# Kernel tuning notes

Measured on AMD Instinct MI355X. Metric: run time of the kernel, lower is better.

The kernel has to match this reference:

```python
import jax, jax.numpy as jnp
import numpy as np

# dims
B, L, H, NH, D = 512, 200, 128, 4, 32      # batch, seq_len, hidden, heads (gnn & fcb), head dim H/NH
FT, TP, IP = 32, 64, 200                    # first_taxonomy_num, taxonomy/item nodes per graph
NHOP, NB = 2, 2                             # n_hop gnn layers, gip_block_nums
SH, FH = 512, 256                           # scb_hidden_units, fcb_hidden_units
ITEMS, TAX = 100001, 2000                   # item vocab (+pad row 0), taxonomy vocab
NT, NI = B * TP, B * IP                     # total taxonomy / item nodes in batched forest
DEG_I, DEG_T = 4, 2                         # in-degree per taxonomy node for i2t / t2t edges


def _ln(x, g, b, eps=1e-8):
    m = jnp.mean(x, -1, keepdims=True)
    v = jnp.mean((x - m) ** 2, -1, keepdims=True)
    return (x - m) / jnp.sqrt(v + eps) * g + b


def _gat(src_h, dst_h, es, ed, W, al, ar, bias):
    """DGL GATConv (eval mode): shared fc, leaky_relu(0.2) scores, segment softmax,
    identity residual (in == heads*out), bias, ReLU activation."""
    fs = (src_h @ W).reshape(-1, NH, D)                 # [Ns,NH,D]
    fd = (dst_h @ W).reshape(-1, NH, D)                 # [Nd,NH,D]
    el = jnp.sum(fs * al, -1)                           # [Ns,NH]
    er = jnp.sum(fd * ar, -1)                           # [Nd,NH]
    e = jax.nn.leaky_relu(el[es] + er[ed], 0.2)         # [E,NH]
    emax = jax.ops.segment_max(e, ed, num_segments=NT)
    a = jnp.exp(e - emax[ed])
    s = jax.ops.segment_sum(a, ed, num_segments=NT)
    alpha = a / s[ed]                                   # [E,NH]
    rst = jax.ops.segment_sum(alpha[..., None] * fs[es], ed, num_segments=NT)
    rst = rst + dst_h.reshape(-1, NH, D) + bias.reshape(NH, D)
    return jax.nn.relu(rst).reshape(-1, NH * D)


def _forward(item_embed, tax_embed, scb_ln_g, scb_ln_b, scb_w1, scb_w2, fcb_ln_g, fcb_ln_b,
             fcb_w1, fcb_w2, fcb_w3, wv, gi_w, gi_al, gi_ar, gi_b, gt_w, gt_al, gt_ar, gt_b,
             liw_g, liw_b, int_g, int_b, uni_w,
             seq, root, i2t_src, i2t_dst, t2t_src, t2t_dst, item_ids, tax_ids):
    # --- global intention: mixer-style blocks over the item sequence ---
    V = item_embed[seq]                                           # [B,L,H]
    for i in range(NB):
        nv = _ln(V, scb_ln_g[i], scb_ln_b[i])
        t = jax.nn.gelu(jnp.einsum('blh,ls->bhs', nv, scb_w1[i]), approximate=False)
        vs = nv + jnp.einsum('bhs,sl->blh', t, scb_w2[i])         # seq-mixing block
        nvs = _ln(vs, fcb_ln_g[i], fcb_ln_b[i])
        xh = nvs.reshape(B, L, NH, D)                             # fcb heads share w1/w2
        y = jax.nn.gelu(jnp.einsum('blkc,cf->blkf', xh, fcb_w1[i]), approximate=False)
        y = jnp.einsum('blkf,fc->blkc', y, fcb_w2[i]).reshape(B, L, H)
        V = nvs + y @ fcb_w3[i]
    alpha = jax.nn.softmax(V @ wv, axis=1)                        # [B,L]
    g = jnp.sum(alpha[..., None] * V, axis=1)                     # [B,H]
    # --- local intention: multi-hop hetero GAT on batched item-taxonomy forest ---
    item_h = item_embed[item_ids]                                 # [NI,H]
    tax_h = tax_embed[tax_ids]                                    # [NT,H]
    acc = jnp.zeros_like(tax_h)
    for hop in range(NHOP):
        t_i = _gat(item_h, tax_h, i2t_src, i2t_dst, gi_w[hop], gi_al[hop], gi_ar[hop], gi_b[hop])
        t_t = _gat(tax_h, tax_h, t2t_src, t2t_dst, gt_w[hop], gt_al[hop], gt_ar[hop], gt_b[hop])
        tax_h = t_i + t_t                                         # HeteroGraphConv 'sum'
        acc = acc + tax_h                                         # k_list accumulation
    total = acc / NHOP                                            # average over hops
    offs = jnp.arange(B) * TP                                     # batched-graph offsets (graph_taxonomy)
    valid = root != -1
    local = jnp.where(valid[..., None], total[jnp.clip(root, 0) + offs[:, None]], 0.0)  # [B,FT,H]
    # --- fuse global + local ---
    mul = jnp.einsum('bfh,bh->bf', local, g)                      # [B,FT]
    w = jax.nn.softmax(jnp.where(mul != 0, _ln(mul, liw_g, liw_b), -jnp.inf), axis=-1)
    intention = _ln(g + jnp.sum(w[..., None] * local, axis=1), int_g, int_b)
    return (intention @ uni_w) @ item_embed.T                     # [B, ITEMS]


def setup_inputs():
    key = jax.random.key(0)
    ks = jax.random.split(key, 32)
    nrm = lambda i, sh: jax.random.normal(ks[i], sh, jnp.float32) * 0.05
    inp = {}
    inp['seq'] = jax.random.randint(ks[0], (B, L), 0, ITEMS)
    inp['root'] = jax.random.randint(ks[1], (B, FT), 0, TP)       # all valid roots
    i2t_dst = jnp.repeat(jnp.arange(NT), DEG_I)
    inp['i2t_dst'] = i2t_dst
    inp['i2t_src'] = (i2t_dst // TP) * IP + jax.random.randint(ks[2], (NT * DEG_I,), 0, IP)
    t2t_dst = jnp.repeat(jnp.arange(NT), DEG_T)
    inp['t2t_dst'] = t2t_dst
    inp['t2t_src'] = (t2t_dst // TP) * TP + jax.random.randint(ks[3], (NT * DEG_T,), 0, TP)
    inp['item_ids'] = jax.random.randint(ks[4], (NI,), 1, ITEMS)
    inp['tax_ids'] = jax.random.randint(ks[5], (NT,), 1, TAX)
    inp['item_embed'] = nrm(6, (ITEMS, H)).at[0].set(0.0)         # padding_idx=0
    inp['tax_embed'] = nrm(7, (TAX, H)).at[0].set(0.0)
    inp['scb_ln_g'] = jnp.ones((NB, H)); inp['scb_ln_b'] = jnp.zeros((NB, H))
    inp['scb_w1'] = nrm(8, (NB, L, SH)); inp['scb_w2'] = nrm(9, (NB, SH, L))
    inp['fcb_ln_g'] = jnp.ones((NB, H)); inp['fcb_ln_b'] = jnp.zeros((NB, H))
    inp['fcb_w1'] = nrm(10, (NB, D, FH)); inp['fcb_w2'] = nrm(11, (NB, FH, D))
    inp['fcb_w3'] = nrm(12, (NB, H, H))
    inp['wv'] = nrm(13, (H,))
    inp['gi_w'] = nrm(14, (NHOP, H, H)); inp['gi_al'] = nrm(15, (NHOP, NH, D))
    inp['gi_ar'] = nrm(16, (NHOP, NH, D)); inp['gi_b'] = nrm(17, (NHOP, H))
    inp['gt_w'] = nrm(18, (NHOP, H, H)); inp['gt_al'] = nrm(19, (NHOP, NH, D))
    inp['gt_ar'] = nrm(20, (NHOP, NH, D)); inp['gt_b'] = nrm(21, (NHOP, H))
    inp['liw_g'] = jnp.ones((FT,)); inp['liw_b'] = jnp.zeros((FT,))
    inp['int_g'] = jnp.ones((H,)); inp['int_b'] = jnp.zeros((H,))
    inp['uni_w'] = nrm(22, (H, H))
    return inp


def reference(item_embed, tax_embed, scb_ln_g, scb_ln_b, scb_w1, scb_w2, fcb_ln_g, fcb_ln_b,
              fcb_w1, fcb_w2, fcb_w3, wv, gi_w, gi_al, gi_ar, gi_b, gt_w, gt_al, gt_ar, gt_b,
              liw_g, liw_b, int_g, int_b, uni_w,
              seq, root, i2t_src, i2t_dst, t2t_src, t2t_dst, item_ids, tax_ids):
    return _forward(item_embed, tax_embed, scb_ln_g, scb_ln_b, scb_w1, scb_w2, fcb_ln_g, fcb_ln_b,
                    fcb_w1, fcb_w2, fcb_w3, wv, gi_w, gi_al, gi_ar, gi_b, gt_w, gt_al, gt_ar, gt_b,
                    liw_g, liw_b, int_g, int_b, uni_w,
                    seq, root, i2t_src, i2t_dst, t2t_src, t2t_dst, item_ids, tax_ids)
```

## Files before the change

### kernel.cpp

```cpp
#include <hip/hip_runtime.h>
#include <hip/hip_bf16.h>

constexpr int TB = 512, TL = 200, TH = 128, TNH = 4, TD = 32;
constexpr int TFT = 32, TTP = 64, TIP = 200;
constexpr int TSH = 512, TFH = 256;
constexpr int TITEMS = 100001;
constexpr int TNT = TB * TTP;
constexpr int TNI = TB * TIP;
constexpr int TLP = 224;
constexpr int TIPAD = 100096;

typedef __attribute__((ext_vector_type(8))) short short8v;
typedef __attribute__((ext_vector_type(4))) float f32x4;

__device__ inline float gelu_exact(float x) {
    return 0.5f * x * (1.0f + erff(x * 0.7071067811865476f));
}
__device__ inline float gelu_fast(float x) {
    float u = x + 0.044715f * x * x * x;
    float e = exp2f(-2.302208f * u);
    return x / (1.0f + e);
}
__device__ inline unsigned short to_bf16u(float x) {
    __hip_bfloat16 h = __float2bfloat16(x);
    return *reinterpret_cast<unsigned short*>(&h);
}
__device__ inline float bfu_to_f(unsigned short u) {
    unsigned int x = ((unsigned int)u) << 16;
    return __uint_as_float(x);
}

__device__ inline float block_reduce_sum(float v, float* red) {
    for (int o = 32; o > 0; o >>= 1) v += __shfl_down(v, o, 64);
    int nw = blockDim.x >> 6;
    if ((threadIdx.x & 63) == 0) red[threadIdx.x >> 6] = v;
    __syncthreads();
    float r = 0.f;
    for (int w = 0; w < nw; ++w) r += red[w];
    __syncthreads();
    return r;
}

__device__ inline float block_reduce_max(float v, float* red) {
    for (int o = 32; o > 0; o >>= 1) v = fmaxf(v, __shfl_down(v, o, 64));
    int nw = blockDim.x >> 6;
    if ((threadIdx.x & 63) == 0) red[threadIdx.x >> 6] = v;
    __syncthreads();
    float r = -INFINITY;
    for (int w = 0; w < nw; ++w) r = fmaxf(r, red[w]);
    __syncthreads();
    return r;
}

__global__ __launch_bounds__(256) void k_gather(const float* __restrict__ tab,
                                                const int* __restrict__ idx,
                                                float* __restrict__ out, int nrows) {
    int e = blockIdx.x * blockDim.x + threadIdx.x;
    if (e >= nrows * 32) return;
    int r = e >> 5, c = e & 31;
    ((float4*)out)[e] = ((const float4*)tab)[(size_t)idx[r] * 32 + c];
}

__global__ __launch_bounds__(256) void k_gather_bf(const float* __restrict__ tab,
                                                   const int* __restrict__ idx,
                                                   unsigned short* __restrict__ out, int nrows) {
    int e = blockIdx.x * blockDim.x + threadIdx.x;
    if (e >= nrows * 16) return;
    int r = e >> 4, c = e & 15;
    const float4 a = ((const float4*)tab)[(size_t)idx[r] * 32 + c * 2];
    const float4 b = ((const float4*)tab)[(size_t)idx[r] * 32 + c * 2 + 1];
    uint4 u;
    u.x = (unsigned int)to_bf16u(a.x) | ((unsigned int)to_bf16u(a.y) << 16);
    u.y = (unsigned int)to_bf16u(a.z) | ((unsigned int)to_bf16u(a.w) << 16);
    u.z = (unsigned int)to_bf16u(b.x) | ((unsigned int)to_bf16u(b.y) << 16);
    u.w = (unsigned int)to_bf16u(b.z) | ((unsigned int)to_bf16u(b.w) << 16);
    *(uint4*)(out + (size_t)e * 8) = u;
}

__global__ __launch_bounds__(256) void k_wcvt(const float* __restrict__ fw1, const float* __restrict__ fw2,
                                              const float* __restrict__ fw3, const float* __restrict__ giw,
                                              const float* __restrict__ gtw, unsigned short* __restrict__ WB) {
    int idx = blockIdx.x * 256 + threadIdx.x;
    float v;
    if (idx < 16384) {
        int nb = idx >> 13, r = idx & 8191, n = r >> 5, k = r & 31;
        v = fw1[(size_t)nb * 8192 + k * 256 + n];
    } else if (idx < 32768) {
        int t = idx - 16384;
        int nb = t >> 13, r = t & 8191, n = r >> 8, k = r & 255;
        v = fw2[(size_t)nb * 8192 + k * 32 + n];
    } else if (idx < 65536) {
        int t = idx - 32768;
        int nb = t >> 14, r = t & 16383, n = r >> 7, k = r & 127;
        v = fw3[(size_t)nb * 16384 + k * 128 + n];
    } else if (idx < 98304) {
        int t = idx - 65536;
        int hop = t >> 14, r = t & 16383, n = r >> 7, k = r & 127;
        v = giw[(size_t)hop * 16384 + k * 128 + n];
    } else {
        int t = idx - 98304;
        int hop = t >> 14, r = t & 16383, n = r >> 7, k = r & 127;
        v = gtw[(size_t)hop * 16384 + k * 128 + n];
    }
    WB[idx] = to_bf16u(v);
}

__global__ __launch_bounds__(256) void k_ln(const float* __restrict__ x, float* __restrict__ y,
                                            const float* __restrict__ g, const float* __restrict__ b) {
    int row = blockIdx.x * 8 + (threadIdx.x >> 5);
    int lane = threadIdx.x & 31;
    const float4 v = ((const float4*)(x + (size_t)row * TH))[lane];
    float s = v.x + v.y + v.z + v.w;
    for (int o = 16; o > 0; o >>= 1) s += __shfl_down(s, o, 32);
    float mean = __shfl(s, 0, 32) * (1.f / 128.f);
    float4 d;
    d.x = v.x - mean; d.y = v.y - mean; d.z = v.z - mean; d.w = v.w - mean;
    float q = d.x * d.x + d.y * d.y + d.z * d.z + d.w * d.w;
    for (int o = 16; o > 0; o >>= 1) q += __shfl_down(q, o, 32);
    float inv = rsqrtf(__shfl(q, 0, 32) * (1.f / 128.f) + 1e-8f);
    const float4 gg = ((const float4*)g)[lane];
    const float4 bb = ((const float4*)b)[lane];
    float4 o4;
    o4.x = d.x * inv * gg.x + bb.x;
    o4.y = d.y * inv * gg.y + bb.y;
    o4.z = d.z * inv * gg.z + bb.z;
    o4.w = d.w * inv * gg.w + bb.w;
    ((float4*)(y + (size_t)row * TH))[lane] = o4;
}

__global__ __launch_bounds__(128) void k_nvt(const float* __restrict__ NV,
                                             unsigned short* __restrict__ NVT) {
    __shared__ float tl[64][129];
    int b = blockIdx.y, l0 = blockIdx.x * 64, tid = threadIdx.x;
    for (int i = tid; i < 2048; i += 128) {
        int r = i >> 5, c = i & 31;
        int l = l0 + r;
        float4 v = {0.f, 0.f, 0.f, 0.f};
        if (l < TL) v = *(const float4*)(NV + ((size_t)b * TL + l) * TH + c * 4);
        tl[r][c * 4 + 0] = v.x; tl[r][c * 4 + 1] = v.y;
        tl[r][c * 4 + 2] = v.z; tl[r][c * 4 + 3] = v.w;
    }
    __syncthreads();
    int h = tid;
    int ng = (l0 + 64 > TLP) ? (TLP - l0) / 8 : 8;
    for (int lg = 0; lg < ng; ++lg) {
        uint4 u;
        unsigned int p[4];
#pragma unroll
        for (int q = 0; q < 4; ++q) {
            unsigned short ua = to_bf16u(tl[lg * 8 + q * 2 + 0][h]);
            unsigned short ub = to_bf16u(tl[lg * 8 + q * 2 + 1][h]);
            p[q] = (unsigned int)ua | ((unsigned int)ub << 16);
        }
        u.x = p[0]; u.y = p[1]; u.z = p[2]; u.w = p[3];
        *(uint4*)(NVT + ((size_t)b * TH + h) * TLP + l0 + lg * 8) = u;
    }
}

__global__ __launch_bounds__(256) void k_wscb(const float* __restrict__ w1, const float* __restrict__ w2,
                                              unsigned short* __restrict__ W1T,
                                              unsigned short* __restrict__ W2T) {
    int bx = blockIdx.x;
    if (bx < TSH) {
        int s = bx, l = threadIdx.x;
        if (l < TLP) W1T[(size_t)s * TLP + l] = to_bf16u(l < TL ? w1[(size_t)l * TSH + s] : 0.f);
    } else {
        int l = bx - TSH;
        for (int it = 0; it < 2; ++it) {
            int s = it * 256 + threadIdx.x;
            W2T[(size_t)l * TSH + s] = to_bf16u(l < TL ? w2[(size_t)s * TL + l] : 0.f);
        }
    }
}

__global__ __launch_bounds__(256) void k_mm1(const unsigned short* __restrict__ NVT,
                                             const unsigned short* __restrict__ W1T,
                                             unsigned short* __restrict__ T, int bh) {
    __shared__ unsigned short As[128][40];
    __shared__ unsigned short Bs[128][40];
    int tid = threadIdx.x;
    int b_local = blockIdx.y, b = bh * 256 + b_local;
    int s0 = blockIdx.x * 128;
    int lane = tid & 63, wid = tid >> 6;
    int mw = wid >> 1, nw = wid & 1;
    f32x4 acc[4][4];
#pragma unroll
    for (int i = 0; i < 4; ++i)
#pragma unroll
        for (int j = 0; j < 4; ++j) acc[i][j] = (f32x4){0.f, 0.f, 0.f, 0.f};
    const unsigned short* Abase = NVT + (size_t)b * TH * TLP;
    const unsigned short* Bbase = W1T + (size_t)s0 * TLP;
    for (int kc = 0; kc < 7; ++kc) {
        __syncthreads();
        for (int i = tid; i < 512; i += 256) {
            int r = i >> 2, q = i & 3;
            *(uint4*)&As[r][q * 8] = *(const uint4*)(Abase + (size_t)r * TLP + kc * 32 + q * 8);
            *(uint4*)&Bs[r][q * 8] = *(const uint4*)(Bbase + (size_t)r * TLP + kc * 32 + q * 8);
        }
        __syncthreads();
        int ko = (lane >> 4) * 8;
        short8v af[4], bfr[4];
#pragma unroll
        for (int t = 0; t < 4; ++t) {
            af[t] = *(const short8v*)&As[mw * 64 + t * 16 + (lane & 15)][ko];
            bfr[t] = *(const short8v*)&Bs[nw * 64 + t * 16 + (lane & 15)][ko];
        }
#pragma unroll
        for (int i = 0; i < 4; ++i)
#pragma unroll
            for (int j = 0; j < 4; ++j)
                acc[i][j] = __builtin_amdgcn_mfma_f32_16x16x32_bf16(af[i], bfr[j], acc[i][j], 0, 0, 0);
    }
    int rbase = (lane >> 4) * 4, col = lane & 15;
#pragma unroll
    for (int i = 0; i < 4; ++i)
#pragma unroll
        for (int j = 0; j < 4; ++j) {
            int h0 = mw * 64 + i * 16 + rbase;
            int s = s0 + nw * 64 + j * 16 + col;
#pragma unroll
            for (int r = 0; r < 4; ++r)
                T[((size_t)b_local * TH + h0 + r) * TSH + s] = to_bf16u(gelu_fast(acc[i][j][r]));
        }
}

__global__ __launch_bounds__(256) void k_mm2(const unsigned short* __restrict__ T,
                                             const unsigned short* __restrict__ W2T,
                                             const float* __restrict__ NV,
                                             float* __restrict__ VS, int bh) {
    __shared__ unsigned short As[128][40];
    __shared__ unsigned short Bs[64][40];
    int tid = threadIdx.x;
    int b_local = blockIdx.y, b = bh * 256 + b_local;
    int l0 = blockIdx.x * 64;
    int lane = tid & 63, wid = tid >> 6;
    f32x4 acc[2][4];
#pragma unroll
    for (int i = 0; i < 2; ++i)
#pragma unroll
        for (int j = 0; j < 4; ++j) acc[i][j] = (f32x4){0.f, 0.f, 0.f, 0.f};
    const unsigned short* Abase = T + (size_t)b_local * TH * TSH;
    for (int kc = 0; kc < 16; ++kc) {
        __syncthreads();
        for (int i = tid; i < 512; i += 256) {
            int r = i >> 2, q = i & 3;
            *(uint4*)&As[r][q * 8] = *(const uint4*)(Abase + (size_t)r * TSH + kc * 32 + q * 8);
        }
        {
            int r = tid >> 2, q = tid & 3;
            int l = l0 + r;
            uint4 v = {0u, 0u, 0u, 0u};
            if (l < 208) v = *(const uint4*)(W2T + (size_t)l * TSH + kc * 32 + q * 8);
            *(uint4*)&Bs[r][q * 8] = v;
        }
        __syncthreads();
        int ko = (lane >> 4) * 8;
        short8v af[2], bfr[4];
#pragma unroll
        for (int t = 0; t < 2; ++t)
            af[t] = *(const short8v*)&As[wid * 32 + t * 16 + (lane & 15)][ko];
#pragma unroll
        for (int j = 0; j < 4; ++j)
            bfr[j] = *(const short8v*)&Bs[j * 16 + (lane & 15)][ko];
#pragma unroll
        for (int i = 0; i < 2; ++i)
#pragma unroll
            for (int j = 0; j < 4; ++j)
                acc[i][j] = __builtin_amdgcn_mfma_f32_16x16x32_bf16(af[i], bfr[j], acc[i][j], 0, 0, 0);
    }
    int rbase = (lane >> 4) * 4, col = lane & 15;
#pragma unroll
    for (int i = 0; i < 2; ++i)
#pragma unroll
        for (int j = 0; j < 4; ++j) {
            int l = l0 + j * 16 + col;
            if (l < TL) {
                int h0 = wid * 32 + i * 16 + rbase;
                size_t off = ((size_t)b * TL + l) * TH + h0;
                const float4 res = *(const float4*)(NV + off);
                float4 o;
                o.x = acc[i][j][0] + res.x;
                o.y = acc[i][j][1] + res.y;
                o.z = acc[i][j][2] + res.z;
                o.w = acc[i][j][3] + res.w;
                *(float4*)(VS + off) = o;
            }
        }
}

__global__ __launch_bounds__(256) void k_ffuse(const float* __restrict__ NV,
                                               const unsigned short* __restrict__ FW1B,
                                               const unsigned short* __restrict__ FW2B,
                                               unsigned short* __restrict__ Z) {
    __shared__ unsigned short As[64][40];
    __shared__ unsigned short BsBuf[256 * 40];
    __shared__ unsigned short Yl[64 * 264];
    int tid = threadIdx.x;
    int m0 = blockIdx.x * 64;
    int lane = tid & 63, wid = tid >> 6;
    for (int i = tid; i < 512; i += 256) {
        int r = i >> 3, q = i & 7;
        const float4 v = *(const float4*)(NV + (size_t)(m0 + r) * 32 + q * 4);
        ushort4 u;
        u.x = to_bf16u(v.x); u.y = to_bf16u(v.y); u.z = to_bf16u(v.z); u.w = to_bf16u(v.w);
        *(ushort4*)&As[r][q * 4] = u;
    }
    for (int i = tid; i < 1024; i += 256) {
        int r = i >> 2, q = i & 3;
        *(uint4*)&BsBuf[r * 40 + q * 8] = *(const uint4*)(FW1B + r * 32 + q * 8);
    }
    __syncthreads();
    int ko = (lane >> 4) * 8;
    short8v af[4], bfr[4];
#pragma unroll
    for (int t = 0; t < 4; ++t) {
        af[t] = *(const short8v*)&As[t * 16 + (lane & 15)][ko];
        bfr[t] = *(const short8v*)&BsBuf[(wid * 64 + t * 16 + (lane & 15)) * 40 + ko];
    }
    __syncthreads();
    {
        f32x4 acc[4][4];
#pragma unroll
        for (int i = 0; i < 4; ++i)
#pragma unroll
            for (int j = 0; j < 4; ++j) acc[i][j] = (f32x4){0.f, 0.f, 0.f, 0.f};
#pragma unroll
        for (int i = 0; i < 4; ++i)
#pragma unroll
            for (int j = 0; j < 4; ++j)
                acc[i][j] = __builtin_amdgcn_mfma_f32_16x16x32_bf16(af[i], bfr[j], acc[i][j], 0, 0, 0);
        int rbase = (lane >> 4) * 4, col = lane & 15;
#pragma unroll
        for (int i = 0; i < 4; ++i)
#pragma unroll
            for (int j = 0; j < 4; ++j)
#pragma unroll
                for (int r = 0; r < 4; ++r) {
                    int m = i * 16 + rbase + r;
                    int n = wid * 64 + j * 16 + col;
                    int idx = (m * 264 + n) ^ (((m >> 2) & 7) << 3);
                    Yl[idx] = to_bf16u(gelu_fast(acc[i][j][r]));
                }
    }
    for (int i = tid; i < 1024; i += 256) {
        int r = i >> 5, q = i & 31;
        *(uint4*)&BsBuf[r * 264 + q * 8] = *(const uint4*)(FW2B + r * 256 + q * 8);
    }
    __syncthreads();
    {
        f32x4 acc2[2];
        acc2[0] = (f32x4){0.f, 0.f, 0.f, 0.f};
        acc2[1] = (f32x4){0.f, 0.f, 0.f, 0.f};
        int mrow = wid * 16 + (lane & 15);
        int sw = ((mrow >> 2) & 7) << 3;
        for (int kc = 0; kc < 8; ++kc) {
            int ko2 = kc * 32 + (lane >> 4) * 8;
            short8v a2 = *(const short8v*)&Yl[(mrow * 264 + ko2) ^ sw];
            short8v b0 = *(const short8v*)&BsBuf[(lane & 15) * 264 + ko2];
            short8v b1 = *(const short8v*)&BsBuf[(16 + (lane & 15)) * 264 + ko2];
            acc2[0] = __builtin_amdgcn_mfma_f32_16x16x32_bf16(a2, b0, acc2[0], 0, 0, 0);
            acc2[1] = __builtin_amdgcn_mfma_f32_16x16x32_bf16(a2, b1, acc2[1], 0, 0, 0);
        }
        int rbase = (lane >> 4) * 4, col = lane & 15;
#pragma unroll
        for (int j = 0; j < 2; ++j)
#pragma unroll
            for (int r = 0; r < 4; ++r)
                Z[(size_t)(m0 + wid * 16 + rbase + r) * 32 + j * 16 + col] =
                    to_bf16u(acc2[j][r]);
    }
}

__global__ __launch_bounds__(256) void k_gmm_b(const unsigned short* __restrict__ A,
                                               const unsigned short* __restrict__ WB,
                                               const float* __restrict__ R,
                                               float* __restrict__ C) {
    __shared__ unsigned short As[128][40];
    __shared__ unsigned short Bs[128][40];
    int tid = threadIdx.x;
    int m0 = blockIdx.x * 128;
    int lane = tid & 63, wid = tid >> 6;
    int mw = wid >> 1, nw = wid & 1;
    f32x4 acc[4][4];
#pragma unroll
    for (int i = 0; i < 4; ++i)
#pragma unroll
        for (int j = 0; j < 4; ++j) acc[i][j] = (f32x4){0.f, 0.f, 0.f, 0.f};
    for (int kc = 0; kc < 4; ++kc) {
        __syncthreads();
        for (int i = tid; i < 512; i += 256) {
            int r = i >> 2, q = i & 3;
            *(uint4*)&As[r][q * 8] = *(const uint4*)(A + (size_t)(m0 + r) * TH + kc * 32 + q * 8);
            *(uint4*)&Bs[r][q * 8] = *(const uint4*)(WB + (size_t)r * TH + kc * 32 + q * 8);
        }
        __syncthreads();
        int ko = (lane >> 4) * 8;
        short8v af[4], bfr[4];
#pragma unroll
        for (int t = 0; t < 4; ++t) {
            af[t] = *(const short8v*)&As[mw * 64 + t * 16 + (lane & 15)][ko];
            bfr[t] = *(const short8v*)&Bs[nw * 64 + t * 16 + (lane & 15)][ko];
        }
#pragma unroll
        for (int i = 0; i < 4; ++i)
#pragma unroll
            for (int j = 0; j < 4; ++j)
                acc[i][j] = __builtin_amdgcn_mfma_f32_16x16x32_bf16(af[i], bfr[j], acc[i][j], 0, 0, 0);
    }
    int rbase = (lane >> 4) * 4, col = lane & 15;
#pragma unroll
    for (int i = 0; i < 4; ++i)
#pragma unroll
        for (int j = 0; j < 4; ++j) {
            int n = nw * 64 + j * 16 + col;
#pragma unroll
            for (int r = 0; r < 4; ++r) {
                size_t off = (size_t)(m0 + mw * 64 + i * 16 + rbase + r) * TH + n;
                float v = acc[i][j][r];
                if (R) v += R[off];
                C[off] = v;
            }
        }
}

__global__ __launch_bounds__(256) void k_pool(const float* __restrict__ V, const float* __restrict__ wv,
                                              float* __restrict__ g) {
    __shared__ float sc[TL];
    __shared__ float red[4];
    int b = blockIdx.x, tid = threadIdx.x;
    if (tid < TL) {
        float a = 0.f;
        const float* vp = V + (size_t)(b * TL + tid) * TH;
        for (int h = 0; h < TH; ++h) a += vp[h] * wv[h];
        sc[tid] = a;
    }
    __syncthreads();
    float m = (tid < TL) ? sc[tid] : -INFINITY;
    m = block_reduce_max(m, red);
    float e = (tid < TL) ? expf(sc[tid] - m) : 0.f;
    float s = block_reduce_sum(e, red);
    if (tid < TL) sc[tid] = e / s;
    __syncthreads();
    if (tid < TH) {
        float a = 0.f;
        for (int l = 0; l < TL; ++l) a += sc[l] * V[(size_t)(b * TL + l) * TH + tid];
        g[b * TH + tid] = a;
    }
}

__global__ __launch_bounds__(256) void k_scores4(
        const float* __restrict__ f0, const float* __restrict__ v0, float* __restrict__ o0, int n0,
        const float* __restrict__ f1, const float* __restrict__ v1, float* __restrict__ o1, int n1,
        const float* __restrict__ f2, const float* __restrict__ v2, float* __restrict__ o2, int n2,
        const float* __restrict__ f3, const float* __restrict__ v3, float* __restrict__ o3, int n3) {
    int t = blockIdx.x * 256 + threadIdx.x;
    const float* f; const float* vec; float* o;
    if (t < n0 * 4) { f = f0; vec = v0; o = o0; }
    else {
        t -= n0 * 4;
        if (t < n1 * 4) { f = f1; vec = v1; o = o1; }
        else {
            t -= n1 * 4;
            if (t < n2 * 4) { f = f2; vec = v2; o = o2; }
            else {
                t -= n2 * 4;
                if (t >= n3 * 4) return;
                f = f3; vec = v3; o = o3;
            }
        }
    }
    int node = t >> 2, k = t & 3;
    const float* fp = f + (size_t)node * TH + k * TD;
    const float* vp = vec + k * TD;
    float a = 0.f;
#pragma unroll
    for (int d = 0; d < TD; ++d) a += fp[d] * vp[d];
    o[t] = a;
}

__global__ __launch_bounds__(128) void k_gat(const unsigned short* __restrict__ tax_cur,
                                             const float* __restrict__ fs_i, const float* __restrict__ el_i,
                                             const float* __restrict__ er_i, const int* __restrict__ src_i,
                                             const float* __restrict__ bi,
                                             const float* __restrict__ fs_t, const float* __restrict__ el_t,
                                             const float* __restrict__ er_t, const int* __restrict__ src_t,
                                             const float* __restrict__ bt,
                                             unsigned short* __restrict__ tax_nxt,
                                             float* __restrict__ acc, int hop) {
    int n = blockIdx.x, h = threadIdx.x, k = h >> 5;
    float cur = bfu_to_f(tax_cur[(size_t)n * TH + h]);
    float ti, tt2;
    {
        float er = er_i[n * 4 + k];
        int s[4]; float e[4]; float m = -INFINITY;
#pragma unroll
        for (int j = 0; j < 4; ++j) {
            s[j] = src_i[n * 4 + j];
            float xx = el_i[s[j] * 4 + k] + er;
            e[j] = xx > 0.f ? xx : 0.2f * xx;
            m = fmaxf(m, e[j]);
        }
        float ssum = 0.f, av = 0.f;
#pragma unroll
        for (int j = 0; j < 4; ++j) {
            float a = expf(e[j] - m);
            ssum += a;
            av += a * fs_i[(size_t)s[j] * TH + h];
        }
        ti = fmaxf(av / ssum + cur + bi[h], 0.f);
    }
    {
        float er = er_t[n * 4 + k];
        int s[2]; float e[2]; float m = -INFINITY;
#pragma unroll
        for (int j = 0; j < 2; ++j) {
            s[j] = src_t[n * 2 + j];
            float xx = el_t[s[j] * 4 + k] + er;
            e[j] = xx > 0.f ? xx : 0.2f * xx;
            m = fmaxf(m, e[j]);
        }
        float ssum = 0.f, av = 0.f;
#pragma unroll
        for (int j = 0; j < 2; ++j) {
            float a = expf(e[j] - m);
            ssum += a;
            av += a * fs_t[(size_t)s[j] * TH + h];
        }
        tt2 = fmaxf(av / ssum + cur + bt[h], 0.f);
    }
    float nx = ti + tt2;
    size_t ai = (size_t)n * TH + h;
    tax_nxt[ai] = to_bf16u(nx);
    acc[ai] = (hop == 0) ? nx : acc[ai] + nx;
}

__global__ __launch_bounds__(128) void k_local(const int* __restrict__ root, const float* __restrict__ acc,
                                               const float* __restrict__ g, float* __restrict__ local,
                                               float* __restrict__ mul) {
    __shared__ float red[2];
    int bf = blockIdx.x, b = bf >> 5;
    int h = threadIdx.x;
    int r = root[bf];
    float v = 0.f;
    if (r != -1) {
        int rc = r < 0 ? 0 : r;
        v = acc[(size_t)(b * TTP + rc) * TH + h] * 0.5f;
    }
    local[(size_t)bf * TH + h] = v;
    float s = block_reduce_sum(v * g[b * TH + h], red);
    if (h == 0) mul[bf] = s;
}

__global__ __launch_bounds__(128) void k_fuse(const float* __restrict__ mul, const float* __restrict__ local,
                                              const float* __restrict__ g,
                                              const float* __restrict__ liw_g, const float* __restrict__ liw_b,
                                              const float* __restrict__ int_g, const float* __restrict__ int_b,
                                              const float* __restrict__ uni_w, unsigned short* __restrict__ PB) {
    __shared__ float lm[TFT], wv_[TFT], inten[TH];
    __shared__ float red[2];
    int b = blockIdx.x, tid = threadIdx.x;
    if (tid < TFT) lm[tid] = mul[b * TFT + tid];
    __syncthreads();
    if (tid < TFT) {
        float mean = 0.f;
        for (int f = 0; f < TFT; ++f) mean += lm[f];
        mean *= (1.f / TFT);
        float var = 0.f;
        for (int f = 0; f < TFT; ++f) { float d = lm[f] - mean; var += d * d; }
        var *= (1.f / TFT);
        float ln = (lm[tid] - mean) * rsqrtf(var + 1e-8f) * liw_g[tid] + liw_b[tid];
        wv_[tid] = (lm[tid] != 0.f) ? ln : -INFINITY;
    }
    __syncthreads();
    if (tid < TFT) {
        float mx = -INFINITY;
        for (int f = 0; f < TFT; ++f) mx = fmaxf(mx, wv_[f]);
        float s = 0.f;
        for (int f = 0; f < TFT; ++f) s += expf(wv_[f] - mx);
        lm[tid] = expf(wv_[tid] - mx) / s;
    }
    __syncthreads();
    float ip = g[b * TH + tid];
    for (int f = 0; f < TFT; ++f) ip += lm[f] * local[(size_t)(b * TFT + f) * TH + tid];
    float mean = block_reduce_sum(ip, red) * (1.f / TH);
    float d = ip - mean;
    float var = block_reduce_sum(d * d, red) * (1.f / TH);
    inten[tid] = d * rsqrtf(var + 1e-8f) * int_g[tid] + int_b[tid];
    __syncthreads();
    float a = 0.f;
    for (int hp = 0; hp < TH; ++hp) a += inten[hp] * uni_w[hp * TH + tid];
    PB[(size_t)b * TH + tid] = to_bf16u(a);
}

__global__ __launch_bounds__(256) void k_ebc(const float* __restrict__ E,
                                             unsigned short* __restrict__ EB) {
    int t = blockIdx.x * 256 + threadIdx.x;
    if (t >= TIPAD * TH / 8) return;
    size_t base = (size_t)t * 8;
    int row = (int)(base >> 7);
    float4 a = {0.f, 0.f, 0.f, 0.f}, b = {0.f, 0.f, 0.f, 0.f};
    if (row < TITEMS) {
        a = *(const float4*)(E + base);
        b = *(const float4*)(E + base + 4);
    }
    ushort4 u0, u1;
    u0.x = to_bf16u(a.x); u0.y = to_bf16u(a.y); u0.z = to_bf16u(a.z); u0.w = to_bf16u(a.w);
    u1.x = to_bf16u(b.x); u1.y = to_bf16u(b.y); u1.z = to_bf16u(b.z); u1.w = to_bf16u(b.w);
    *(ushort4*)(EB + base) = u0;
    *(ushort4*)(EB + base + 4) = u1;
}

__global__ __launch_bounds__(256) void k_final_m(const unsigned short* __restrict__ PB,
                                                 const unsigned short* __restrict__ EB,
                                                 float* __restrict__ out) {
    __shared__ unsigned short As[128][136];
    __shared__ unsigned short Bs[128][136];
    int tid = threadIdx.x;
    int i0 = blockIdx.x * 128, b0 = blockIdx.y * 128;
    for (int i = tid; i < 2048; i += 256) {
        int r = i >> 4, q = i & 15;
        *(uint4*)&As[r][q * 8] = *(const uint4*)(PB + (size_t)(b0 + r) * TH + q * 8);
    }
    for (int i = tid; i < 2048; i += 256) {
        int r = i >> 4, q = i & 15;
        *(uint4*)&Bs[r][q * 8] = *(const uint4*)(EB + (size_t)(i0 + r) * TH + q * 8);
    }
    __syncthreads();
    int lane = tid & 63, wid = tid >> 6;
    int mw = wid >> 1, nw = wid & 1;
    f32x4 acc[4][4];
#pragma unroll
    for (int i = 0; i < 4; ++i)
#pragma unroll
        for (int j = 0; j < 4; ++j) acc[i][j] = (f32x4){0.f, 0.f, 0.f, 0.f};
#pragma unroll
    for (int kc = 0; kc < 4; ++kc) {
        int ko = kc * 32 + (lane >> 4) * 8;
        short8v af[4], bfr[4];
#pragma unroll
        for (int t = 0; t < 4; ++t) {
            af[t] = *(const short8v*)&As[mw * 64 + t * 16 + (lane & 15)][ko];
            bfr[t] = *(const short8v*)&Bs[nw * 64 + t * 16 + (lane & 15)][ko];
        }
#pragma unroll
        for (int i = 0; i < 4; ++i)
#pragma unroll
            for (int j = 0; j < 4; ++j)
                acc[i][j] = __builtin_amdgcn_mfma_f32_16x16x32_bf16(af[i], bfr[j], acc[i][j], 0, 0, 0);
    }
    int rbase = (lane >> 4) * 4, col = lane & 15;
#pragma unroll
    for (int i = 0; i < 4; ++i)
#pragma unroll
        for (int j = 0; j < 4; ++j) {
            int ii = i0 + nw * 64 + j * 16 + col;
            if (ii < TITEMS) {
#pragma unroll
                for (int r = 0; r < 4; ++r)
                    out[(size_t)(b0 + mw * 64 + i * 16 + rbase + r) * TITEMS + ii] = acc[i][j][r];
            }
        }
}

extern "C" void kernel_launch(void* const* d_in, const int* in_sizes, int n_in,
                              void* d_out, int out_size, void* d_ws, size_t ws_size,
                              hipStream_t stream) {
    const int*   seq        = (const int*)d_in[0];
    const int*   root       = (const int*)d_in[1];
    const int*   i2t_src    = (const int*)d_in[3];
    const int*   t2t_src    = (const int*)d_in[5];
    const int*   item_ids   = (const int*)d_in[6];
    const int*   tax_ids    = (const int*)d_in[7];
    const float* item_embed = (const float*)d_in[8];
    const float* tax_embed  = (const float*)d_in[9];
    const float* scb_ln_g   = (const float*)d_in[10];
    const float* scb_ln_b   = (const float*)d_in[11];
    const float* scb_w1     = (const float*)d_in[12];
    const float* scb_w2     = (const float*)d_in[13];
    const float* fcb_ln_g   = (const float*)d_in[14];
    const float* fcb_ln_b   = (const float*)d_in[15];
    const float* fcb_w1     = (const float*)d_in[16];
    const float* fcb_w2     = (const float*)d_in[17];
    const float* fcb_w3     = (const float*)d_in[18];
    const float* wv         = (const float*)d_in[19];
    const float* gi_w       = (const float*)d_in[20];
    const float* gi_al      = (const float*)d_in[21];
    const float* gi_ar      = (const float*)d_in[22];
    const float* gi_b       = (const float*)d_in[23];
    const float* gt_w       = (const float*)d_in[24];
    const float* gt_al      = (const float*)d_in[25];
    const float* gt_ar      = (const float*)d_in[26];
    const float* gt_b       = (const float*)d_in[27];
    const float* liw_g      = (const float*)d_in[28];
    const float* liw_b      = (const float*)d_in[29];
    const float* int_g      = (const float*)d_in[30];
    const float* int_b      = (const float*)d_in[31];
    const float* uni_w      = (const float*)d_in[32];

    char* w = (char*)d_ws;
    float* V     = (float*)(w + 0);
    float* NV    = (float*)(w + 52428800);
    float* FSI   = V;
    unsigned short* ITEMHB = (unsigned short*)(w + 52428800);
    unsigned short* NVT = (unsigned short*)(w + 104857600);
    unsigned short* T   = (unsigned short*)(w + 134217728);
    unsigned short* W1T = (unsigned short*)(w + 167772160);
    unsigned short* W2T = (unsigned short*)(w + 168001536);
    unsigned short* ZB  = (unsigned short*)(w + 104857600);
    unsigned short* TAXB0 = (unsigned short*)(w + 104857600);
    unsigned short* TAXB1 = (unsigned short*)(w + 113246208);
    float* ACC   = (float*)(w + 138412032);
    float* FDI   = (float*)(w + 155189248);
    float* FST   = (float*)(w + 171966464);
    float* ELI   = (float*)(w + 188743680);
    float* ERI   = (float*)(w + 190382080);
    float* ELT   = (float*)(w + 190906368);
    float* ERT   = (float*)(w + 191430656);
    float* LOCAL = (float*)(w + 191954944);
    float* G     = (float*)(w + 200343552);
    float* MUL   = (float*)(w + 200605696);
    unsigned short* WB = (unsigned short*)(w + 191954944);
    unsigned short* EB = (unsigned short*)(w + 155189248);
    unsigned short* PB = (unsigned short*)(w + 200671232);
    if (ws_size < 200933376ull) return;

    k_wcvt<<<512, 256, 0, stream>>>(fcb_w1, fcb_w2, fcb_w3, gi_w, gt_w, WB);

    k_gather<<<(TB * TL * 32 + 255) / 256, 256, 0, stream>>>(item_embed, seq, V, TB * TL);
    for (int nb = 0; nb < 2; ++nb) {
        k_ln<<<TB * TL / 8, 256, 0, stream>>>(V, NV, scb_ln_g + nb * TH, scb_ln_b + nb * TH);
        k_nvt<<<dim3(4, TB), 128, 0, stream>>>(NV, NVT);
        k_wscb<<<720, 256, 0, stream>>>(scb_w1 + nb * TL * TSH, scb_w2 + nb * TSH * TL, W1T, W2T);
        for (int bh = 0; bh < 2; ++bh) {
            k_mm1<<<dim3(4, 256), 256, 0, stream>>>(NVT, W1T, T, bh);
            k_mm2<<<dim3(4, 256), 256, 0, stream>>>(T, W2T, NV, V, bh);
        }
        k_ln<<<TB * TL / 8, 256, 0, stream>>>(V, NV, fcb_ln_g + nb * TH, fcb_ln_b + nb * TH);
        k_ffuse<<<TB * TL * 4 / 64, 256, 0, stream>>>(NV, WB + nb * 8192, WB + 16384 + nb * 8192, ZB);
        k_gmm_b<<<TB * TL / 128, 256, 0, stream>>>(ZB, WB + 32768 + nb * 16384, NV, V);
    }
    k_pool<<<TB, 256, 0, stream>>>(V, wv, G);

    k_gather_bf<<<(TNI * 16 + 255) / 256, 256, 0, stream>>>(item_embed, item_ids, ITEMHB, TNI);
    k_gather_bf<<<(TNT * 16 + 255) / 256, 256, 0, stream>>>(tax_embed, tax_ids, TAXB0, TNT);

    unsigned short* curb = TAXB0;
    unsigned short* nxtb = TAXB1;
    for (int hop = 0; hop < 2; ++hop) {
        const unsigned short* WiB = WB + 65536 + hop * 16384;
        const unsigned short* WtB = WB + 98304 + hop * 16384;
        k_gmm_b<<<TNI / 128, 256, 0, stream>>>(ITEMHB, WiB, nullptr, FSI);
        k_gmm_b<<<TNT / 128, 256, 0, stream>>>(curb, WiB, nullptr, FDI);
        k_gmm_b<<<TNT / 128, 256, 0, stream>>>(curb, WtB, nullptr, FST);
        int total = (TNI + 3 * TNT) * TNH;
        k_scores4<<<(total + 255) / 256, 256, 0, stream>>>(
            FSI, gi_al + hop * TH, ELI, TNI,
            FDI, gi_ar + hop * TH, ERI, TNT,
            FST, gt_al + hop * TH, ELT, TNT,
            FST, gt_ar + hop * TH, ERT, TNT);
        k_gat<<<TNT, 128, 0, stream>>>(curb, FSI, ELI, ERI, i2t_src, gi_b + hop * TH,
                                       FST, ELT, ERT, t2t_src, gt_b + hop * TH, nxtb, ACC, hop);
        unsigned short* tmp = curb; curb = nxtb; nxtb = tmp;
    }

    k_local<<<TB * TFT, 128, 0, stream>>>(root, ACC, G, LOCAL, MUL);
    k_fuse<<<TB, 128, 0, stream>>>(MUL, LOCAL, G, liw_g, liw_b, int_g, int_b, uni_w, PB);
    k_ebc<<<(TIPAD * TH / 8 + 255) / 256, 256, 0, stream>>>(item_embed, EB);
    k_final_m<<<dim3(TIPAD / 128, TB / 128), 256, 0, stream>>>(PB, EB, (float*)d_out);
}
```

Measured before the change: 1.030 ms.

## Fuse layernorms into transpose and mm2, store GAT features as bf16

The SCB layernorm is merged with the bf16 transpose kernel, and the FCB layernorm is folded into the mm2 epilogue through a shared-memory staging tile. The GAT projection GEMMs now write bf16 instead of fp32, which halves traffic for the score and aggregation kernels. k_local and k_fuse become one kernel, and k_final_m reads PB directly from global memory instead of staging it in LDS. Together these remove several launches and full-tensor round trips, at the cost of lower feature precision, a single-pass variance formula, and more shared memory in mm2l.

```diff
diff --git a/kernel.cpp b/kernel.cpp
--- a/kernel.cpp
+++ b/kernel.cpp
@@ -13,9 +13,6 @@
 typedef __attribute__((ext_vector_type(8))) short short8v;
 typedef __attribute__((ext_vector_type(4))) float f32x4;
 
-__device__ inline float gelu_exact(float x) {
-    return 0.5f * x * (1.0f + erff(x * 0.7071067811865476f));
-}
 __device__ inline float gelu_fast(float x) {
     float u = x + 0.044715f * x * x * x;
     float e = exp2f(-2.302208f * u);
@@ -37,17 +34,6 @@
     __syncthreads();
     float r = 0.f;
     for (int w = 0; w < nw; ++w) r += red[w];
-    __syncthreads();
-    return r;
-}
-
-__device__ inline float block_reduce_max(float v, float* red) {
-    for (int o = 32; o > 0; o >>= 1) v = fmaxf(v, __shfl_down(v, o, 64));
-    int nw = blockDim.x >> 6;
-    if ((threadIdx.x & 63) == 0) red[threadIdx.x >> 6] = v;
-    __syncthreads();
-    float r = -INFINITY;
-    for (int w = 0; w < nw; ++w) r = fmaxf(r, red[w]);
     __syncthreads();
     return r;
 }
@@ -105,40 +91,53 @@
     WB[idx] = to_bf16u(v);
 }
 
-__global__ __launch_bounds__(256) void k_ln(const float* __restrict__ x, float* __restrict__ y,
-                                            const float* __restrict__ g, const float* __restrict__ b) {
-    int row = blockIdx.x * 8 + (threadIdx.x >> 5);
-    int lane = threadIdx.x & 31;
-    const float4 v = ((const float4*)(x + (size_t)row * TH))[lane];
-    float s = v.x + v.y + v.z + v.w;
-    for (int o = 16; o > 0; o >>= 1) s += __shfl_down(s, o, 32);
-    float mean = __shfl(s, 0, 32) * (1.f / 128.f);
-    float4 d;
-    d.x = v.x - mean; d.y = v.y - mean; d.z = v.z - mean; d.w = v.w - mean;
-    float q = d.x * d.x + d.y * d.y + d.z * d.z + d.w * d.w;
-    for (int o = 16; o > 0; o >>= 1) q += __shfl_down(q, o, 32);
-    float inv = rsqrtf(__shfl(q, 0, 32) * (1.f / 128.f) + 1e-8f);
-    const float4 gg = ((const float4*)g)[lane];
-    const float4 bb = ((const float4*)b)[lane];
-    float4 o4;
-    o4.x = d.x * inv * gg.x + bb.x;
-    o4.y = d.y * inv * gg.y + bb.y;
-    o4.z = d.z * inv * gg.z + bb.z;
-    o4.w = d.w * inv * gg.w + bb.w;
-    ((float4*)(y + (size_t)row * TH))[lane] = o4;
-}
-
-__global__ __launch_bounds__(128) void k_nvt(const float* __restrict__ NV,
-                                             unsigned short* __restrict__ NVT) {
+__global__ __launch_bounds__(128) void k_lnt(const float* __restrict__ V,
+                                             const float* __restrict__ g, const float* __restrict__ b,
+                                             float* __restrict__ NV, unsigned short* __restrict__ NVT) {
     __shared__ float tl[64][129];
-    int b = blockIdx.y, l0 = blockIdx.x * 64, tid = threadIdx.x;
+    __shared__ float mrow[64], irow[64];
+    int bb = blockIdx.y, l0 = blockIdx.x * 64, tid = threadIdx.x;
     for (int i = tid; i < 2048; i += 128) {
         int r = i >> 5, c = i & 31;
         int l = l0 + r;
         float4 v = {0.f, 0.f, 0.f, 0.f};
-        if (l < TL) v = *(const float4*)(NV + ((size_t)b * TL + l) * TH + c * 4);
+        if (l < TL) v = *(const float4*)(V + ((size_t)bb * TL + l) * TH + c * 4);
         tl[r][c * 4 + 0] = v.x; tl[r][c * 4 + 1] = v.y;
         tl[r][c * 4 + 2] = v.z; tl[r][c * 4 + 3] = v.w;
+    }
+    __syncthreads();
+    {
+        int row = tid >> 1, half = tid & 1;
+        float s = 0.f, sq = 0.f;
+        for (int k = 0; k < 64; ++k) {
+            float v = tl[row][half * 64 + k];
+            s += v; sq += v * v;
+        }
+        s += __shfl_xor(s, 1);
+        sq += __shfl_xor(sq, 1);
+        if (half == 0) {
+            float mean = s * (1.f / 128.f);
+            mrow[row] = mean;
+            irow[row] = rsqrtf(sq * (1.f / 128.f) - mean * mean + 1e-8f);
+        }
+    }
+    __syncthreads();
+    for (int i = tid; i < 2048; i += 128) {
+        int r = i >> 5, c = i & 31;
+        int l = l0 + r;
+        float4 o = {0.f, 0.f, 0.f, 0.f};
+        if (l < TL) {
+            float4 v = *(float4*)&tl[r][c * 4];
+            float m = mrow[r], inv = irow[r];
+            const float4 gg = ((const float4*)g)[c];
+            const float4 bv = ((const float4*)b)[c];
+            o.x = (v.x - m) * inv * gg.x + bv.x;
+            o.y = (v.y - m) * inv * gg.y + bv.y;
+            o.z = (v.z - m) * inv * gg.z + bv.z;
+            o.w = (v.w - m) * inv * gg.w + bv.w;
+            *(float4*)(NV + ((size_t)bb * TL + l) * TH + c * 4) = o;
+        }
+        *(float4*)&tl[r][c * 4] = o;
     }
     __syncthreads();
     int h = tid;
@@ -153,7 +152,7 @@
             p[q] = (unsigned int)ua | ((unsigned int)ub << 16);
         }
         u.x = p[0]; u.y = p[1]; u.z = p[2]; u.w = p[3];
-        *(uint4*)(NVT + ((size_t)b * TH + h) * TLP + l0 + lg * 8) = u;
+        *(uint4*)(NVT + ((size_t)bb * TH + h) * TLP + l0 + lg * 8) = u;
     }
 }
 
@@ -224,12 +223,15 @@
         }
 }
 
-__global__ __launch_bounds__(256) void k_mm2(const unsigned short* __restrict__ T,
-                                             const unsigned short* __restrict__ W2T,
-                                             const float* __restrict__ NV,
-                                             float* __restrict__ VS, int bh) {
+__global__ __launch_bounds__(256) void k_mm2l(const unsigned short* __restrict__ T,
+                                              const unsigned short* __restrict__ W2T,
+                                              float* __restrict__ NV,
+                                              const float* __restrict__ lg, const float* __restrict__ lb,
+                                              int bh) {
     __shared__ unsigned short As[128][40];
     __shared__ unsigned short Bs[64][40];
+    __shared__ float vsl[64][132];
+    __shared__ float mrow[64], irow[64];
     int tid = threadIdx.x;
     int b_local = blockIdx.y, b = bh * 256 + b_local;
     int l0 = blockIdx.x * 64;
@@ -274,18 +276,50 @@
 #pragma unroll
         for (int j = 0; j < 4; ++j) {
             int l = l0 + j * 16 + col;
-            if (l < TL) {
-                int h0 = wid * 32 + i * 16 + rbase;
-                size_t off = ((size_t)b * TL + l) * TH + h0;
-                const float4 res = *(const float4*)(NV + off);
+            int h0 = wid * 32 + i * 16 + rbase;
+            float4 res = {0.f, 0.f, 0.f, 0.f};
+            if (l < TL) res = *(const float4*)(NV + ((size_t)b * TL + l) * TH + h0);
+            vsl[j * 16 + col][h0 + 0] = acc[i][j][0] + res.x;
+            vsl[j * 16 + col][h0 + 1] = acc[i][j][1] + res.y;
+            vsl[j * 16 + col][h0 + 2] = acc[i][j][2] + res.z;
+            vsl[j * 16 + col][h0 + 3] = acc[i][j][3] + res.w;
+        }
+    __syncthreads();
+    int row = tid >> 2, q = tid & 3;
+    {
+        float s = 0.f, sq = 0.f;
+        for (int k = 0; k < 32; ++k) {
+            float v = vsl[row][q * 32 + k];
+            s += v; sq += v * v;
+        }
+        s += __shfl_xor(s, 1); s += __shfl_xor(s, 2);
+        sq += __shfl_xor(sq, 1); sq += __shfl_xor(sq, 2);
+        if (q == 0) {
+            float mean = s * (1.f / 128.f);
+            mrow[row] = mean;
+            irow[row] = rsqrtf(sq * (1.f / 128.f) - mean * mean + 1e-8f);
+        }
+    }
+    __syncthreads();
+    {
+        int l = l0 + row;
+        if (l < TL) {
+            float mean = mrow[row], inv = irow[row];
+            float* dst = NV + ((size_t)b * TL + l) * TH + q * 32;
+#pragma unroll
+            for (int k4 = 0; k4 < 8; ++k4) {
+                float4 v = *(float4*)&vsl[row][q * 32 + k4 * 4];
+                const float4 gg = ((const float4*)lg)[q * 8 + k4];
+                const float4 bv = ((const float4*)lb)[q * 8 + k4];
                 float4 o;
-                o.x = acc[i][j][0] + res.x;
-                o.y = acc[i][j][1] + res.y;
-                o.z = acc[i][j][2] + res.z;
-                o.w = acc[i][j][3] + res.w;
-                *(float4*)(VS + off) = o;
+                o.x = (v.x - mean) * inv * gg.x + bv.x;
+                o.y = (v.y - mean) * inv * gg.y + bv.y;
+                o.z = (v.z - mean) * inv * gg.z + bv.z;
+                o.w = (v.w - mean) * inv * gg.w + bv.w;
+                *(float4*)(dst + k4 * 4) = o;
             }
         }
+    }
 }
 
 __global__ __launch_bounds__(256) void k_ffuse(const float* __restrict__ NV,
@@ -423,6 +457,55 @@
         }
 }
 
+__global__ __launch_bounds__(256) void k_gmm_bb(const unsigned short* __restrict__ A,
+                                                const unsigned short* __restrict__ WB,
+                                                unsigned short* __restrict__ C) {
+    __shared__ unsigned short As[128][40];
+    __shared__ unsigned short Bs[128][40];
+    int tid = threadIdx.x;
+    int m0 = blockIdx.x * 128;
+    int lane = tid & 63, wid = tid >> 6;
+    int mw = wid >> 1, nw = wid & 1;
+    f32x4 acc[4][4];
+#pragma unroll
+    for (int i = 0; i < 4; ++i)
+#pragma unroll
+        for (int j = 0; j < 4; ++j) acc[i][j] = (f32x4){0.f, 0.f, 0.f, 0.f};
+    for (int kc = 0; kc < 4; ++kc) {
+        __syncthreads();
+        for (int i = tid; i < 512; i += 256) {
+            int r = i >> 2, q = i & 3;
+            *(uint4*)&As[r][q * 8] = *(const uint4*)(A + (size_t)(m0 + r) * TH + kc * 32 + q * 8);
+            *(uint4*)&Bs[r][q * 8] = *(const uint4*)(WB + (size_t)r * TH + kc * 32 + q * 8);
+        }
+        __syncthreads();
+        int ko = (lane >> 4) * 8;
+        short8v af[4], bfr[4];
+#pragma unroll
+        for (int t = 0; t < 4; ++t) {
+            af[t] = *(const short8v*)&As[mw * 64 + t * 16 + (lane & 15)][ko];
+            bfr[t] = *(const short8v*)&Bs[nw * 64 + t * 16 + (lane & 15)][ko];
+        }
+#pragma unroll
+        for (int i = 0; i < 4; ++i)
+#pragma unroll
+            for (int j = 0; j < 4; ++j)
+                acc[i][j] = __builtin_amdgcn_mfma_f32_16x16x32_bf16(af[i], bfr[j], acc[i][j], 0, 0, 0);
+    }
+    int rbase = (lane >> 4) * 4, col = lane & 15;
+#pragma unroll
+    for (int i = 0; i < 4; ++i)
+#pragma unroll
+        for (int j = 0; j < 4; ++j) {
+            int n = nw * 64 + j * 16 + col;
+#pragma unroll
+            for (int r = 0; r < 4; ++r) {
+                size_t off = (size_t)(m0 + mw * 64 + i * 16 + rbase + r) * TH + n;
+                C[off] = to_bf16u(acc[i][j][r]);
+            }
+        }
+}
+
 __global__ __launch_bounds__(256) void k_pool(const float* __restrict__ V, const float* __restrict__ wv,
                                               float* __restrict__ g) {
     __shared__ float sc[TL];
@@ -436,7 +519,11 @@
     }
     __syncthreads();
     float m = (tid < TL) ? sc[tid] : -INFINITY;
-    m = block_reduce_max(m, red);
+    for (int o = 32; o > 0; o >>= 1) m = fmaxf(m, __shfl_down(m, o, 64));
+    if ((tid & 63) == 0) red[tid >> 6] = m;
+    __syncthreads();
+    m = fmaxf(fmaxf(red[0], red[1]), fmaxf(red[2], red[3]));
+    __syncthreads();
     float e = (tid < TL) ? expf(sc[tid] - m) : 0.f;
     float s = block_reduce_sum(e, red);
     if (tid < TL) sc[tid] = e / s;
@@ -449,12 +536,12 @@
 }
 
 __global__ __launch_bounds__(256) void k_scores4(
-        const float* __restrict__ f0, const float* __restrict__ v0, float* __restrict__ o0, int n0,
-        const float* __restrict__ f1, const float* __restrict__ v1, float* __restrict__ o1, int n1,
-        const float* __restrict__ f2, const float* __restrict__ v2, float* __restrict__ o2, int n2,
-        const float* __restrict__ f3, const float* __restrict__ v3, float* __restrict__ o3, int n3) {
+        const unsigned short* __restrict__ f0, const float* __restrict__ v0, float* __restrict__ o0, int n0,
+        const unsigned short* __restrict__ f1, const float* __restrict__ v1, float* __restrict__ o1, int n1,
+        const unsigned short* __restrict__ f2, const float* __restrict__ v2, float* __restrict__ o2, int n2,
+        const unsigned short* __restrict__ f3, const float* __restrict__ v3, float* __restrict__ o3, int n3) {
     int t = blockIdx.x * 256 + threadIdx.x;
-    const float* f; const float* vec; float* o;
+    const unsigned short* f; const float* vec; float* o;
     if (t < n0 * 4) { f = f0; vec = v0; o = o0; }
     else {
         t -= n0 * 4;
@@ -470,19 +557,27 @@
         }
     }
     int node = t >> 2, k = t & 3;
-    const float* fp = f + (size_t)node * TH + k * TD;
+    const unsigned short* fp = f + (size_t)node * TH + k * TD;
     const float* vp = vec + k * TD;
     float a = 0.f;
 #pragma unroll
-    for (int d = 0; d < TD; ++d) a += fp[d] * vp[d];
+    for (int q = 0; q < 4; ++q) {
+        uint4 u = *(const uint4*)(fp + q * 8);
+        unsigned int ws[4] = {u.x, u.y, u.z, u.w};
+#pragma unroll
+        for (int p = 0; p < 4; ++p) {
+            a += __uint_as_float(ws[p] << 16) * vp[q * 8 + p * 2];
+            a += __uint_as_float(ws[p] & 0xffff0000u) * vp[q * 8 + p * 2 + 1];
+        }
+    }
     o[t] = a;
 }
 
 __global__ __launch_bounds__(128) void k_gat(const unsigned short* __restrict__ tax_cur,
-                                             const float* __restrict__ fs_i, const float* __restrict__ el_i,
+                                             const unsigned short* __restrict__ fs_i, const float* __restrict__ el_i,
                                              const float* __restrict__ er_i, const int* __restrict__ src_i,
                                              const float* __restrict__ bi,
-                                             const float* __restrict__ fs_t, const float* __restrict__ el_t,
+                                             const unsigned short* __restrict__ fs_t, const float* __restrict__ el_t,
                                              const float* __restrict__ er_t, const int* __restrict__ src_t,
                                              const float* __restrict__ bt,
                                              unsigned short* __restrict__ tax_nxt,
@@ -505,7 +600,7 @@
         for (int j = 0; j < 4; ++j) {
             float a = expf(e[j] - m);
             ssum += a;
-            av += a * fs_i[(size_t)s[j] * TH + h];
+            av += a * bfu_to_f(fs_i[(size_t)s[j] * TH + h]);
         }
         ti = fmaxf(av / ssum + cur + bi[h], 0.f);
     }
@@ -524,7 +619,7 @@
         for (int j = 0; j < 2; ++j) {
             float a = expf(e[j] - m);
             ssum += a;
-            av += a * fs_t[(size_t)s[j] * TH + h];
+            av += a * bfu_to_f(fs_t[(size_t)s[j] * TH + h]);
         }
         tt2 = fmaxf(av / ssum + cur + bt[h], 0.f);
     }
@@ -534,32 +629,25 @@
     acc[ai] = (hop == 0) ? nx : acc[ai] + nx;
 }
 
-__global__ __launch_bounds__(128) void k_local(const int* __restrict__ root, const float* __restrict__ acc,
-                                               const float* __restrict__ g, float* __restrict__ local,
-                                               float* __restrict__ mul) {
-    __shared__ float red[2];
-    int bf = blockIdx.x, b = bf >> 5;
-    int h = threadIdx.x;
-    int r = root[bf];
-    float v = 0.f;
-    if (r != -1) {
-        int rc = r < 0 ? 0 : r;
-        v = acc[(size_t)(b * TTP + rc) * TH + h] * 0.5f;
-    }
-    local[(size_t)bf * TH + h] = v;
-    float s = block_reduce_sum(v * g[b * TH + h], red);
-    if (h == 0) mul[bf] = s;
-}
-
-__global__ __launch_bounds__(128) void k_fuse(const float* __restrict__ mul, const float* __restrict__ local,
-                                              const float* __restrict__ g,
-                                              const float* __restrict__ liw_g, const float* __restrict__ liw_b,
-                                              const float* __restrict__ int_g, const float* __restrict__ int_b,
-                                              const float* __restrict__ uni_w, unsigned short* __restrict__ PB) {
+__global__ __launch_bounds__(128) void k_locfuse(const int* __restrict__ root, const float* __restrict__ acc,
+                                                 const float* __restrict__ g,
+                                                 const float* __restrict__ liw_g, const float* __restrict__ liw_b,
+                                                 const float* __restrict__ int_g, const float* __restrict__ int_b,
+                                                 const float* __restrict__ uni_w,
+                                                 unsigned short* __restrict__ PB) {
+    __shared__ float loc[TFT][TH];
     __shared__ float lm[TFT], wv_[TFT], inten[TH];
     __shared__ float red[2];
     int b = blockIdx.x, tid = threadIdx.x;
-    if (tid < TFT) lm[tid] = mul[b * TFT + tid];
+    float gv = g[b * TH + tid];
+    for (int f = 0; f < TFT; ++f) {
+        int r = root[b * TFT + f];
+        float v = 0.f;
+        if (r != -1) v = acc[(size_t)(b * TTP + (r < 0 ? 0 : r)) * TH + tid] * 0.5f;
+        loc[f][tid] = v;
+        float s = block_reduce_sum(v * gv, red);
+        if (tid == 0) lm[f] = s;
+    }
     __syncthreads();
     if (tid < TFT) {
         float mean = 0.f;
@@ -580,8 +668,8 @@
         lm[tid] = expf(wv_[tid] - mx) / s;
     }
     __syncthreads();
-    float ip = g[b * TH + tid];
-    for (int f = 0; f < TFT; ++f) ip += lm[f] * local[(size_t)(b * TFT + f) * TH + tid];
+    float ip = gv;
+    for (int f = 0; f < TFT; ++f) ip += lm[f] * loc[f][tid];
     float mean = block_reduce_sum(ip, red) * (1.f / TH);
     float d = ip - mean;
     float var = block_reduce_sum(d * d, red) * (1.f / TH);
@@ -613,16 +701,11 @@
 __global__ __launch_bounds__(256) void k_final_m(const unsigned short* __restrict__ PB,
                                                  const unsigned short* __restrict__ EB,
                                                  float* __restrict__ out) {
-    __shared__ unsigned short As[128][136];
     __shared__ unsigned short Bs[128][136];
     int tid = threadIdx.x;
     int i0 = blockIdx.x * 128, b0 = blockIdx.y * 128;
     for (int i = tid; i < 2048; i += 256) {
         int r = i >> 4, q = i & 15;
-        *(uint4*)&As[r][q * 8] = *(const uint4*)(PB + (size_t)(b0 + r) * TH + q * 8);
-    }
-    for (int i = tid; i < 2048; i += 256) {
-        int r = i >> 4, q = i & 15;
         *(uint4*)&Bs[r][q * 8] = *(const uint4*)(EB + (size_t)(i0 + r) * TH + q * 8);
     }
     __syncthreads();
@@ -639,7 +722,7 @@
         short8v af[4], bfr[4];
 #pragma unroll
         for (int t = 0; t < 4; ++t) {
-            af[t] = *(const short8v*)&As[mw * 64 + t * 16 + (lane & 15)][ko];
+            af[t] = *(const short8v*)(PB + (size_t)(b0 + mw * 64 + t * 16 + (lane & 15)) * TH + ko);
             bfr[t] = *(const short8v*)&Bs[nw * 64 + t * 16 + (lane & 15)][ko];
         }
 #pragma unroll
@@ -700,7 +783,7 @@
     char* w = (char*)d_ws;
     float* V     = (float*)(w + 0);
     float* NV    = (float*)(w + 52428800);
-    float* FSI   = V;
+    unsigned short* FSIB   = (unsigned short*)(w + 0);
     unsigned short* ITEMHB = (unsigned short*)(w + 52428800);
     unsigned short* NVT = (unsigned short*)(w + 104857600);
     unsigned short* T   = (unsigned short*)(w + 134217728);
@@ -710,15 +793,13 @@
     unsigned short* TAXB0 = (unsigned short*)(w + 104857600);
     unsigned short* TAXB1 = (unsigned short*)(w + 113246208);
     float* ACC   = (float*)(w + 138412032);
-    float* FDI   = (float*)(w + 155189248);
-    float* FST   = (float*)(w + 171966464);
+    unsigned short* FDIB = (unsigned short*)(w + 155189248);
+    unsigned short* FSTB = (unsigned short*)(w + 171966464);
     float* ELI   = (float*)(w + 188743680);
     float* ERI   = (float*)(w + 190382080);
     float* ELT   = (float*)(w + 190906368);
     float* ERT   = (float*)(w + 191430656);
-    float* LOCAL = (float*)(w + 191954944);
     float* G     = (float*)(w + 200343552);
-    float* MUL   = (float*)(w + 200605696);
     unsigned short* WB = (unsigned short*)(w + 191954944);
     unsigned short* EB = (unsigned short*)(w + 155189248);
     unsigned short* PB = (unsigned short*)(w + 200671232);
@@ -728,14 +809,13 @@
 
     k_gather<<<(TB * TL * 32 + 255) / 256, 256, 0, stream>>>(item_embed, seq, V, TB * TL);
     for (int nb = 0; nb < 2; ++nb) {
-        k_ln<<<TB * TL / 8, 256, 0, stream>>>(V, NV, scb_ln_g + nb * TH, scb_ln_b + nb * TH);
-        k_nvt<<<dim3(4, TB), 128, 0, stream>>>(NV, NVT);
+        k_lnt<<<dim3(4, TB), 128, 0, stream>>>(V, scb_ln_g + nb * TH, scb_ln_b + nb * TH, NV, NVT);
         k_wscb<<<720, 256, 0, stream>>>(scb_w1 + nb * TL * TSH, scb_w2 + nb * TSH * TL, W1T, W2T);
         for (int bh = 0; bh < 2; ++bh) {
             k_mm1<<<dim3(4, 256), 256, 0, stream>>>(NVT, W1T, T, bh);
-            k_mm2<<<dim3(4, 256), 256, 0, stream>>>(T, W2T, NV, V, bh);
-        }
-        k_ln<<<TB * TL / 8, 256, 0, stream>>>(V, NV, fcb_ln_g + nb * TH, fcb_ln_b + nb * TH);
+            k_mm2l<<<dim3(4, 256), 256, 0, stream>>>(T, W2T, NV,
+                                                     fcb_ln_g + nb * TH, fcb_ln_b + nb * TH, bh);
+        }
         k_ffuse<<<TB * TL * 4 / 64, 256, 0, stream>>>(NV, WB + nb * 8192, WB + 16384 + nb * 8192, ZB);
         k_gmm_b<<<TB * TL / 128, 256, 0, stream>>>(ZB, WB + 32768 + nb * 16384, NV, V);
     }
@@ -749,22 +829,21 @@
     for (int hop = 0; hop < 2; ++hop) {
         const unsigned short* WiB = WB + 65536 + hop * 16384;
         const unsigned short* WtB = WB + 98304 + hop * 16384;
-        k_gmm_b<<<TNI / 128, 256, 0, stream>>>(ITEMHB, WiB, nullptr, FSI);
-        k_gmm_b<<<TNT / 128, 256, 0, stream>>>(curb, WiB, nullptr, FDI);
-        k_gmm_b<<<TNT / 128, 256, 0, stream>>>(curb, WtB, nullptr, FST);
+        k_gmm_bb<<<TNI / 128, 256, 0, stream>>>(ITEMHB, WiB, FSIB);
+        k_gmm_bb<<<TNT / 128, 256, 0, stream>>>(curb, WiB, FDIB);
+        k_gmm_bb<<<TNT / 128, 256, 0, stream>>>(curb, WtB, FSTB);
         int total = (TNI + 3 * TNT) * TNH;
         k_scores4<<<(total + 255) / 256, 256, 0, stream>>>(
-            FSI, gi_al + hop * TH, ELI, TNI,
-            FDI, gi_ar + hop * TH, ERI, TNT,
-            FST, gt_al + hop * TH, ELT, TNT,
-            FST, gt_ar + hop * TH, ERT, TNT);
-        k_gat<<<TNT, 128, 0, stream>>>(curb, FSI, ELI, ERI, i2t_src, gi_b + hop * TH,
-                                       FST, ELT, ERT, t2t_src, gt_b + hop * TH, nxtb, ACC, hop);
+            FSIB, gi_al + hop * TH, ELI, TNI,
+            FDIB, gi_ar + hop * TH, ERI, TNT,
+            FSTB, gt_al + hop * TH, ELT, TNT,
+            FSTB, gt_ar + hop * TH, ERT, TNT);
+        k_gat<<<TNT, 128, 0, stream>>>(curb, FSIB, ELI, ERI, i2t_src, gi_b + hop * TH,
+                                       FSTB, ELT, ERT, t2t_src, gt_b + hop * TH, nxtb, ACC, hop);
         unsigned short* tmp = curb; curb = nxtb; nxtb = tmp;
     }
 
-    k_local<<<TB * TFT, 128, 0, stream>>>(root, ACC, G, LOCAL, MUL);
-    k_fuse<<<TB, 128, 0, stream>>>(MUL, LOCAL, G, liw_g, liw_b, int_g, int_b, uni_w, PB);
+    k_locfuse<<<TB, 128, 0, stream>>>(root, ACC, G, liw_g, liw_b, int_g, int_b, uni_w, PB);
     k_ebc<<<(TIPAD * TH / 8 + 255) / 256, 256, 0, stream>>>(item_embed, EB);
     k_final_m<<<dim3(TIPAD / 128, TB / 128), 256, 0, stream>>>(PB, EB, (float*)d_out);
 }
```

New measurement: 1.033 ms. About the same (+0.3%).
